# Kernel tuning notes

Hardware: AMD Instinct MI355X
Metric: run time of the kernel (lower is better)

Reference implementation:

```python
import jax, jax.numpy as jnp
import numpy as np

C, H1, H2, K, HOUT = 128, 4, 5, 3, 4  # h_dim, gat1 heads, gat2 heads, BAN k, BAN h_out
BN_EPS = 1e-5


def _gat(x, W, a_src, a_dst, bias, src, dst, mask, N):
    # PyG-style GATConv: x:[N,Fin], W:[Fin,H*C], a_*:[H,C], mask:[E] (1=valid edge)
    H, Ch = a_src.shape
    xh = (x @ W).reshape(N, H, Ch)
    es = jnp.einsum('nhc,hc->nh', xh, a_src)
    ed = jnp.einsum('nhc,hc->nh', xh, a_dst)
    e = jax.nn.leaky_relu(es[src] + ed[dst], 0.2)                      # [E,H]
    e = jnp.where(mask[:, None] > 0, e, -1e9)
    m = jax.ops.segment_max(e, dst, num_segments=N)                    # [N,H]
    p = jnp.exp(e - m[dst]) * mask[:, None]
    s = jax.ops.segment_sum(p, dst, num_segments=N)
    alpha = p / s[dst]                                                 # segment softmax over incoming edges
    out = jax.ops.segment_sum(xh[src] * alpha[:, :, None], dst, num_segments=N)
    return out.reshape(N, H * Ch) + bias


def _forward(cell_features, Wd, bd, W1, a1s, a1d, b1, Wl1, bl1, W2, a2s, a2d, b2, Wl2, bl2,
             Wfc, bfc, Whg, bhg, Wc, bc, Wv, bv, Wq, bq, h_mat, h_bias, bn_gamma, bn_beta,
             triplets, edge_index):
    N = triplets.shape[0]
    src0, dst0 = edge_index[0], edge_index[1]
    # clean_edge_index drops self loops; GATConv (PyG default) re-adds exactly one per node
    idx = jnp.arange(N, dtype=src0.dtype)
    src = jnp.concatenate([src0, idx])
    dst = jnp.concatenate([dst0, idx])
    mask = jnp.concatenate([(src0 != dst0).astype(jnp.float32), jnp.ones((N,), jnp.float32)])
    x = triplets[:, :4].astype(jnp.float32) @ Wd + bd                  # drug_linear
    h1 = jax.nn.elu(_gat(x, W1, a1s, a1d, b1, src, dst, mask, N)) @ Wl1 + bl1
    h2 = jax.nn.elu(_gat(h1, W2, a2s, a2d, b2, src, dst, mask, N)) @ Wl2 + bl2
    h = jnp.mean(h1 + h2, axis=0)                                      # [C] graph readout
    hg = jax.nn.relu(h @ Wfc + bfc) @ Whg + bhg                        # [C]
    c = jax.nn.relu(cell_features @ Wc + bc)                           # [B,C]
    B = c.shape[0]
    v = jnp.broadcast_to(hg, (B, C))
    # BANLayer (DrugBAN) with singleton v/q sequence length
    v_ = jax.nn.relu(v @ Wv + bv)                                      # [B,C*K]
    q_ = jax.nn.relu(c @ Wq + bq)
    att = jnp.einsum('hk,bk,bk->bh', h_mat, v_, q_) + h_bias           # [B,HOUT]
    fused = att.sum(axis=1, keepdims=True) * (v_ * q_)                 # sum over heads of bilinear pooling
    logits = fused.reshape(B, C, K).sum(axis=-1)                       # AvgPool1d(k)*k == group sum
    mu = logits.mean(axis=0)
    var = logits.var(axis=0)                                           # biased var, as torch BN
    return (logits - mu) / jnp.sqrt(var + BN_EPS) * bn_gamma + bn_beta


def setup_inputs():
    key = jax.random.key(0)
    ks = iter(jax.random.split(key, 40))
    N, E, B, CF = 20000, 500000, 256, 954
    def w(shape, fan):
        return jax.random.normal(next(ks), shape, jnp.float32) / np.sqrt(fan)
    return dict(
        cell_features=jax.random.normal(next(ks), (B, CF), jnp.float32),
        Wd=w((4, C), 4), bd=jnp.zeros((C,), jnp.float32),
        W1=w((C, H1 * C), C), a1s=w((H1, C), C), a1d=w((H1, C), C), b1=jnp.zeros((H1 * C,), jnp.float32),
        Wl1=w((H1 * C, C), H1 * C), bl1=jnp.zeros((C,), jnp.float32),
        W2=w((C, H2 * C), C), a2s=w((H2, C), C), a2d=w((H2, C), C), b2=jnp.zeros((H2 * C,), jnp.float32),
        Wl2=w((H2 * C, C), H2 * C), bl2=jnp.zeros((C,), jnp.float32),
        Wfc=w((C, 2 * C), C), bfc=jnp.zeros((2 * C,), jnp.float32),
        Whg=w((2 * C, C), 2 * C), bhg=jnp.zeros((C,), jnp.float32),
        Wc=w((CF, C), CF), bc=jnp.zeros((C,), jnp.float32),
        Wv=w((C, C * K), C), bv=jnp.zeros((C * K,), jnp.float32),
        Wq=w((C, C * K), C), bq=jnp.zeros((C * K,), jnp.float32),
        h_mat=w((HOUT, C * K), C * K), h_bias=jnp.zeros((HOUT,), jnp.float32),
        bn_gamma=jnp.ones((C,), jnp.float32), bn_beta=jnp.zeros((C,), jnp.float32),
        triplets=jax.random.randint(next(ks), (N, 4), 0, 10, dtype=jnp.int32),
        edge_index=jax.random.randint(next(ks), (2, E), 0, N, dtype=jnp.int32),
    )


def reference(cell_features, Wd, bd, W1, a1s, a1d, b1, Wl1, bl1, W2, a2s, a2d, b2, Wl2, bl2,
              Wfc, bfc, Whg, bhg, Wc, bc, Wv, bv, Wq, bq, h_mat, h_bias, bn_gamma, bn_beta,
              triplets, edge_index):
    return _forward(cell_features, Wd, bd, W1, a1s, a1d, b1, Wl1, bl1, W2, a2s, a2d, b2, Wl2, bl2,
                    Wfc, bfc, Whg, bhg, Wc, bc, Wv, bv, Wq, bq, h_mat, h_bias, bn_gamma, bn_beta,
                    triplets, edge_index)
```

## Files before the change

kernel.cpp:

```cpp
#include <hip/hip_runtime.h>
#include <hip/hip_bf16.h>
#include <math.h>

#define CDIV(a,b) (((a)+(b)-1)/(b))

typedef __attribute__((ext_vector_type(8))) short short8v;
typedef __attribute__((ext_vector_type(4))) float f32x4;

__device__ inline float bf2lo(unsigned u) { return __uint_as_float(u << 16); }
__device__ inline float bf2hi(unsigned u) { return __uint_as_float(u & 0xffff0000u); }
__device__ inline float leaky(float v) { return v > 0.f ? v : 0.2f * v; }

__global__ void k_prep(const float* __restrict__ W1, __hip_bfloat16* __restrict__ W1t,
                       const float* __restrict__ Wl1, __hip_bfloat16* __restrict__ Wl1t,
                       const float* __restrict__ W2, __hip_bfloat16* __restrict__ W2t,
                       const float* __restrict__ Wl2, __hip_bfloat16* __restrict__ Wl2t,
                       const float* __restrict__ Wc, float* __restrict__ Wct,
                       const float* __restrict__ Wq, float* __restrict__ Wqt,
                       float* __restrict__ colsum, int* __restrict__ degz,
                       float* __restrict__ esz, int N) {
  int i = blockIdx.x * 256 + threadIdx.x;
  const int n1 = 128 * 512, n2 = 512 * 128, n3 = 128 * 640, n4 = 640 * 128;
  const int n5 = 954 * 128, n6 = 128 * 384;
  if (i < n1) { int m = i / 128, k = i % 128; W1t[i] = __float2bfloat16(W1[(size_t)k * 512 + m]); return; }
  i -= n1;
  if (i < n2) { int m = i / 512, k = i % 512; Wl1t[i] = __float2bfloat16(Wl1[(size_t)k * 128 + m]); return; }
  i -= n2;
  if (i < n3) { int m = i / 128, k = i % 128; W2t[i] = __float2bfloat16(W2[(size_t)k * 640 + m]); return; }
  i -= n3;
  if (i < n4) { int m = i / 640, k = i % 640; Wl2t[i] = __float2bfloat16(Wl2[(size_t)k * 128 + m]); return; }
  i -= n4;
  if (i < n5) { int m = i / 954, k = i % 954; Wct[i] = Wc[(size_t)k * 128 + m]; return; }
  i -= n5;
  if (i < n6) { int m = i / 128, k = i % 128; Wqt[i] = Wq[(size_t)k * 384 + m]; return; }
  i -= n6;
  if (i < 128) { colsum[i] = 0.f; return; }
  i -= 128;
  if (i < 2 * N) { degz[i] = 0; return; }
  i -= 2 * N;
  if (i < 18 * N) { esz[i] = 0.f; return; }
}

__global__ void k_degdrug(const int* __restrict__ src0, const int* __restrict__ dst0,
                          int* __restrict__ deg, int E,
                          const int* __restrict__ trip, const float* __restrict__ Wd,
                          const float* __restrict__ bd, __hip_bfloat16* __restrict__ x,
                          int N) {
  int i = blockIdx.x * 256 + threadIdx.x;
  if (i < E) {
    int s = src0[i], d = dst0[i];
    if (s != d) atomicAdd(&deg[d], 1);
    return;
  }
  i -= E;
  if (i >= N * 128) return;
  int n = i >> 7, c = i & 127;
  const int* t = trip + n * 4;
  float acc = bd[c];
  acc += (float)t[0] * Wd[c] + (float)t[1] * Wd[128 + c] +
         (float)t[2] * Wd[256 + c] + (float)t[3] * Wd[384 + c];
  x[i] = __float2bfloat16(acc);
}

template <bool BIAS, bool COLSUM, bool COEF>
__global__ void k_gemm_mfma(const __hip_bfloat16* __restrict__ A,
                            const __hip_bfloat16* __restrict__ Bt,
                            const float* __restrict__ bias,
                            __hip_bfloat16* __restrict__ Cb,
                            float* __restrict__ colsum,
                            const float* __restrict__ as_, const float* __restrict__ ad_,
                            float* __restrict__ es, float* __restrict__ ed,
                            int Nr, int K, int M) {
  __shared__ short As[64 * 40];
  __shared__ short Bs[64 * 40];
  int tid = threadIdx.x;
  int lane = tid & 63, wid = tid >> 6;
  int wr = wid >> 1, wc = wid & 1;
  int lrow = lane & 15;
  int row0 = blockIdx.y * 64, col0 = blockIdx.x * 64;

  int arow = tid >> 2, akc = tid & 3;
  int grow = row0 + arow; if (grow >= Nr) grow = Nr - 1;
  const __hip_bfloat16* agp = A + (size_t)grow * K + akc * 8;
  const __hip_bfloat16* bgp = Bt + (size_t)(col0 + arow) * K + akc * 8;
  short* asp = &As[arow * 40 + akc * 8];
  short* bsp = &Bs[arow * 40 + akc * 8];

  f32x4 acc00 = {0.f,0.f,0.f,0.f}, acc01 = acc00, acc10 = acc00, acc11 = acc00;

  int lkc = lane >> 4;
  const short* a0p = &As[(wr * 32 + lrow) * 40 + lkc * 8];
  const short* a1p = &As[(wr * 32 + 16 + lrow) * 40 + lkc * 8];
  const short* b0p = &Bs[(wc * 32 + lrow) * 40 + lkc * 8];
  const short* b1p = &Bs[(wc * 32 + 16 + lrow) * 40 + lkc * 8];

  short8v av = *(const short8v*)agp;
  short8v bv = *(const short8v*)bgp;
  for (int k0 = 0; k0 < K; k0 += 32) {
    __syncthreads();
    *(short8v*)asp = av;
    *(short8v*)bsp = bv;
    __syncthreads();
    if (k0 + 32 < K) {
      av = *(const short8v*)(agp + k0 + 32);
      bv = *(const short8v*)(bgp + k0 + 32);
    }
    short8v a0 = *(const short8v*)a0p;
    short8v a1 = *(const short8v*)a1p;
    short8v b0 = *(const short8v*)b0p;
    short8v b1 = *(const short8v*)b1p;
    acc00 = __builtin_amdgcn_mfma_f32_16x16x32_bf16(a0, b0, acc00, 0, 0, 0);
    acc01 = __builtin_amdgcn_mfma_f32_16x16x32_bf16(a0, b1, acc01, 0, 0, 0);
    acc10 = __builtin_amdgcn_mfma_f32_16x16x32_bf16(a1, b0, acc10, 0, 0, 0);
    acc11 = __builtin_amdgcn_mfma_f32_16x16x32_bf16(a1, b1, acc11, 0, 0, 0);
  }

  int rbase = row0 + wr * 32 + (lane >> 4) * 4;
  int cbase = col0 + wc * 32 + lrow;
  int hplane = col0 >> 7;
  float part0 = 0.f, part1 = 0.f;
  float esp[2][4], edp[2][4];
  float as0, as1, ad0, ad1;
  if (COEF) {
#pragma unroll
    for (int m = 0; m < 2; ++m)
#pragma unroll
      for (int r = 0; r < 4; ++r) { esp[m][r] = 0.f; edp[m][r] = 0.f; }
    int ch0 = (cbase & 127);
    as0 = as_[hplane * 128 + ch0];
    as1 = as_[hplane * 128 + ch0 + 16];
    ad0 = ad_[hplane * 128 + ch0];
    ad1 = ad_[hplane * 128 + ch0 + 16];
  }
#pragma unroll
  for (int m = 0; m < 2; ++m) {
#pragma unroll
    for (int n = 0; n < 2; ++n) {
      f32x4 acc = m == 0 ? (n == 0 ? acc00 : acc01) : (n == 0 ? acc10 : acc11);
      int col = cbase + n * 16;
      int plane = col >> 7, ch = col & 127;
      float bv2 = BIAS ? bias[col] : 0.f;
      __hip_bfloat16* cp = Cb + (size_t)plane * Nr * 128 + ch;
#pragma unroll
      for (int r = 0; r < 4; ++r) {
        int grow2 = rbase + m * 16 + r;
        if (grow2 >= Nr) continue;
        float v = acc[r] + bv2;
        cp[(size_t)grow2 * 128] = __float2bfloat16(v);
        if (COLSUM) { if (n == 0) part0 += v; else part1 += v; }
        if (COEF) {
          esp[m][r] += v * (n == 0 ? as0 : as1);
          edp[m][r] += v * (n == 0 ? ad0 : ad1);
        }
      }
    }
  }
  if (COLSUM) {
    part0 += __shfl_xor(part0, 16); part0 += __shfl_xor(part0, 32);
    part1 += __shfl_xor(part1, 16); part1 += __shfl_xor(part1, 32);
    if (lane < 16) {
      atomicAdd(&colsum[cbase], part0);
      atomicAdd(&colsum[cbase + 16], part1);
    }
  }
  if (COEF) {
#pragma unroll
    for (int m = 0; m < 2; ++m) {
#pragma unroll
      for (int r = 0; r < 4; ++r) {
        float e = esp[m][r], d = edp[m][r];
        e += __shfl_xor(e, 1); e += __shfl_xor(e, 2);
        e += __shfl_xor(e, 4); e += __shfl_xor(e, 8);
        d += __shfl_xor(d, 1); d += __shfl_xor(d, 2);
        d += __shfl_xor(d, 4); d += __shfl_xor(d, 8);
        if ((lane & 15) == 0) {
          int grow2 = rbase + m * 16 + r;
          if (grow2 < Nr) {
            atomicAdd(&es[(size_t)hplane * Nr + grow2], e);
            atomicAdd(&ed[(size_t)hplane * Nr + grow2], d);
          }
        }
      }
    }
  }
}

__global__ void k_dotmm(const float* __restrict__ A, const float* __restrict__ Bt,
                        const float* __restrict__ bias, float* __restrict__ C,
                        int Nr, int K, int M) {
  int wid = (blockIdx.x * blockDim.x + threadIdx.x) >> 6;
  int lane = threadIdx.x & 63;
  if (wid >= Nr * M) return;
  int b = wid / M, m = wid % M;
  const float* ar = A + (size_t)b * K;
  const float* br = Bt + (size_t)m * K;
  float acc = 0.f;
  for (int k = lane * 2; k + 1 < K; k += 128) {
    float2 av = *(const float2*)(ar + k);
    float2 bv = *(const float2*)(br + k);
    acc += av.x * bv.x + av.y * bv.y;
  }
#pragma unroll
  for (int off = 32; off; off >>= 1) acc += __shfl_xor(acc, off);
  if (lane == 0) C[wid] = fmaxf(acc + bias[m], 0.f);
}

__global__ void k_scan(const int* __restrict__ deg, int* __restrict__ rowptr, int N) {
  __shared__ int part[1024];
  int t = threadIdx.x;
  int chunk = (N + 1023) >> 10;
  int b0 = t * chunk, b1 = min(N, b0 + chunk);
  int s = 0;
  for (int i = b0; i < b1; i++) s += deg[i];
  part[t] = s;
  __syncthreads();
  for (int off = 1; off < 1024; off <<= 1) {
    int v = (t >= off) ? part[t - off] : 0;
    __syncthreads();
    part[t] += v;
    __syncthreads();
  }
  int run = (t == 0) ? 0 : part[t - 1];
  for (int i = b0; i < b1; i++) { rowptr[i] = run; run += deg[i]; }
  if (b1 == N) rowptr[N] = run;
}

__global__ void k_fill_adj(const int* __restrict__ src0, const int* __restrict__ dst0,
                           const int* __restrict__ rowptr, int* __restrict__ cursor,
                           int* __restrict__ adj, int E) {
  int e = blockIdx.x * 256 + threadIdx.x;
  if (e >= E) return;
  int s = src0[e], d = dst0[e];
  if (s != d) {
    int pos = rowptr[d] + atomicAdd(&cursor[d], 1);
    adj[pos] = s;
  }
}

__device__ __forceinline__ void acc8p(const char* xbase, int loff, unsigned pk, int j,
                                      float& a0, float& a1) {
  unsigned k0 = __builtin_amdgcn_readlane(pk, j);
  unsigned k1 = __builtin_amdgcn_readlane(pk, j + 1);
  unsigned k2 = __builtin_amdgcn_readlane(pk, j + 2);
  unsigned k3 = __builtin_amdgcn_readlane(pk, j + 3);
  unsigned k4 = __builtin_amdgcn_readlane(pk, j + 4);
  unsigned k5 = __builtin_amdgcn_readlane(pk, j + 5);
  unsigned k6 = __builtin_amdgcn_readlane(pk, j + 6);
  unsigned k7 = __builtin_amdgcn_readlane(pk, j + 7);
  unsigned u0 = *(const unsigned*)(xbase + (size_t)(k0 & 0x7FFFu) * 256 + loff);
  unsigned u1 = *(const unsigned*)(xbase + (size_t)(k1 & 0x7FFFu) * 256 + loff);
  unsigned u2 = *(const unsigned*)(xbase + (size_t)(k2 & 0x7FFFu) * 256 + loff);
  unsigned u3 = *(const unsigned*)(xbase + (size_t)(k3 & 0x7FFFu) * 256 + loff);
  unsigned u4 = *(const unsigned*)(xbase + (size_t)(k4 & 0x7FFFu) * 256 + loff);
  unsigned u5 = *(const unsigned*)(xbase + (size_t)(k5 & 0x7FFFu) * 256 + loff);
  unsigned u6 = *(const unsigned*)(xbase + (size_t)(k6 & 0x7FFFu) * 256 + loff);
  unsigned u7 = *(const unsigned*)(xbase + (size_t)(k7 & 0x7FFFu) * 256 + loff);
  float p0 = __uint_as_float(k0 & 0xFFFF0000u);
  float p1 = __uint_as_float(k1 & 0xFFFF0000u);
  float p2 = __uint_as_float(k2 & 0xFFFF0000u);
  float p3 = __uint_as_float(k3 & 0xFFFF0000u);
  float p4 = __uint_as_float(k4 & 0xFFFF0000u);
  float p5 = __uint_as_float(k5 & 0xFFFF0000u);
  float p6 = __uint_as_float(k6 & 0xFFFF0000u);
  float p7 = __uint_as_float(k7 & 0xFFFF0000u);
  a0 += p0 * bf2lo(u0); a1 += p0 * bf2hi(u0);
  a0 += p1 * bf2lo(u1); a1 += p1 * bf2hi(u1);
  a0 += p2 * bf2lo(u2); a1 += p2 * bf2hi(u2);
  a0 += p3 * bf2lo(u3); a1 += p3 * bf2hi(u3);
  a0 += p4 * bf2lo(u4); a1 += p4 * bf2hi(u4);
  a0 += p5 * bf2lo(u5); a1 += p5 * bf2hi(u5);
  a0 += p6 * bf2lo(u6); a1 += p6 * bf2hi(u6);
  a0 += p7 * bf2lo(u7); a1 += p7 * bf2hi(u7);
}

__global__ void k_gat_gather(const int* __restrict__ rowptr, const int* __restrict__ adj,
                             const float* __restrict__ es, const float* __restrict__ ed,
                             const __hip_bfloat16* __restrict__ xh,
                             const float* __restrict__ bias,
                             __hip_bfloat16* __restrict__ gout, int N, int H) {
  int nb = gridDim.x, bx = blockIdx.x;
  int sb = ((nb & 7) == 0) ? ((bx & 7) * (nb >> 3) + (bx >> 3)) : bx;
  int h = blockIdx.y;
  int n = sb * 4 + (threadIdx.x >> 6);
  int lane = threadIdx.x & 63;
  if (n >= N) return;
  int base = rowptr[n];
  int deg = rowptr[n + 1] - base;
  const float* esh = es + (size_t)h * N;
  float edn = ed[(size_t)h * N + n];
  float vself = leaky(esh[n] + edn);
  const char* xbase = (const char*)xh + (size_t)h * N * 256;
  int loff = lane * 4;

  float a0 = 0.f, a1 = 0.f;
  float psum = 0.f, pself, m;

  if (deg <= 64) {
    int s = 0; float v = -3e38f;
    if (lane < deg) { s = adj[base + lane]; v = leaky(esh[s] + edn); }
    m = fmaxf(vself, v);
#pragma unroll
    for (int off = 32; off; off >>= 1) m = fmaxf(m, __shfl_xor(m, off));
    float p = (lane < deg) ? __expf(v - m) : 0.f;
    pself = __expf(vself - m);
    psum = p;
    unsigned pk = (__float_as_uint(p) & 0xFFFF0000u) | (unsigned)s;
    for (int j = 0; j < deg; j += 8) acc8p(xbase, loff, pk, j, a0, a1);
  } else {
    m = vself;
    for (int i = lane; i < deg; i += 64) {
      int s = adj[base + i];
      m = fmaxf(m, leaky(esh[s] + edn));
    }
#pragma unroll
    for (int off = 32; off; off >>= 1) m = fmaxf(m, __shfl_xor(m, off));
    pself = __expf(vself - m);
    for (int c = 0; c < deg; c += 64) {
      int i = c + lane;
      int s = 0; float p = 0.f;
      if (i < deg) {
        s = adj[base + i];
        p = __expf(leaky(esh[s] + edn) - m);
        psum += p;
      }
      unsigned pk = (__float_as_uint(p) & 0xFFFF0000u) | (unsigned)s;
      int cnt = min(64, deg - c);
      for (int j = 0; j < cnt; j += 8) acc8p(xbase, loff, pk, j, a0, a1);
    }
  }

  {
    unsigned u = *(const unsigned*)(xbase + (size_t)n * 256 + loff);
    a0 += pself * bf2lo(u);
    a1 += pself * bf2hi(u);
  }
#pragma unroll
  for (int off = 32; off; off >>= 1) psum += __shfl_xor(psum, off);
  psum += pself;
  float inv = 1.f / psum;
  float2 bv = ((const float2*)(bias + h * 128))[lane];
  float o0 = a0 * inv + bv.x;
  float o1 = a1 * inv + bv.y;
  o0 = o0 > 0.f ? o0 : __expf(o0) - 1.f;
  o1 = o1 > 0.f ? o1 : __expf(o1) - 1.f;
  __hip_bfloat162 r;
  r.x = __float2bfloat16(o0);
  r.y = __float2bfloat16(o1);
  ((__hip_bfloat162*)(gout + (size_t)n * (H * 128) + h * 128))[lane] = r;
}

__global__ void k_head(const float* __restrict__ colsum, const float* __restrict__ Wfc,
                       const float* __restrict__ bfc, const float* __restrict__ Whg,
                       const float* __restrict__ bhg, const float* __restrict__ Wv,
                       const float* __restrict__ bv, float* __restrict__ vvec, float invN) {
  __shared__ float h[128], t1[256], hg[128];
  int t = threadIdx.x;
  if (t < 128) h[t] = colsum[t] * invN;
  __syncthreads();
  float acc = bfc[t];
  for (int k = 0; k < 128; k++) acc += h[k] * Wfc[k * 256 + t];
  t1[t] = fmaxf(acc, 0.f);
  __syncthreads();
  if (t < 128) {
    float a2 = bhg[t];
    for (int k = 0; k < 256; k++) a2 += t1[k] * Whg[k * 128 + t];
    hg[t] = a2;
  }
  __syncthreads();
  for (int j = t; j < 384; j += 256) {
    float a3 = bv[j];
    for (int k = 0; k < 128; k++) a3 += hg[k] * Wv[k * 384 + j];
    vvec[j] = fmaxf(a3, 0.f);
  }
}

__global__ void k_fused(const float* __restrict__ vvec, const float* __restrict__ q,
                        const float* __restrict__ hmat, const float* __restrict__ hbias,
                        float* __restrict__ logits) {
  int b = blockIdx.x, c = threadIdx.x;
  __shared__ float red[128];
  float t[3];
  float part = 0.f;
#pragma unroll
  for (int j = 0; j < 3; j++) {
    int k = c * 3 + j;
    float hs = hmat[k] + hmat[384 + k] + hmat[768 + k] + hmat[1152 + k];
    t[j] = vvec[k] * q[(size_t)b * 384 + k];
    part += hs * t[j];
  }
  red[c] = part;
  __syncthreads();
  for (int s = 64; s > 0; s >>= 1) {
    if (c < s) red[c] += red[c + s];
    __syncthreads();
  }
  float attsum = red[0] + (hbias[0] + hbias[1] + hbias[2] + hbias[3]);
  logits[(size_t)b * 128 + c] = attsum * (t[0] + t[1] + t[2]);
}

__global__ void k_bn(const float* __restrict__ logits, const float* __restrict__ gamma,
                     const float* __restrict__ beta, float* __restrict__ out, int B) {
  int c = blockIdx.x, b = threadIdx.x;
  __shared__ float s1[256], s2[256];
  float v = logits[(size_t)b * 128 + c];
  s1[b] = v; s2[b] = v * v;
  __syncthreads();
  for (int s = B / 2; s > 0; s >>= 1) {
    if (b < s) { s1[b] += s1[b + s]; s2[b] += s2[b + s]; }
    __syncthreads();
  }
  float mu = s1[0] / B;
  float var = s2[0] / B - mu * mu;
  out[(size_t)b * 128 + c] = (v - mu) * rsqrtf(var + 1e-5f) * gamma[c] + beta[c];
}

extern "C" void kernel_launch(void* const* d_in, const int* in_sizes, int n_in,
                              void* d_out, int out_size, void* d_ws, size_t ws_size,
                              hipStream_t stream) {
  const float* cell = (const float*)d_in[0];
  const float* Wd   = (const float*)d_in[1];
  const float* bd   = (const float*)d_in[2];
  const float* W1   = (const float*)d_in[3];
  const float* a1s  = (const float*)d_in[4];
  const float* a1d  = (const float*)d_in[5];
  const float* b1   = (const float*)d_in[6];
  const float* Wl1  = (const float*)d_in[7];
  const float* bl1  = (const float*)d_in[8];
  const float* W2   = (const float*)d_in[9];
  const float* a2s  = (const float*)d_in[10];
  const float* a2d  = (const float*)d_in[11];
  const float* b2   = (const float*)d_in[12];
  const float* Wl2  = (const float*)d_in[13];
  const float* bl2  = (const float*)d_in[14];
  const float* Wfc  = (const float*)d_in[15];
  const float* bfc  = (const float*)d_in[16];
  const float* Whg  = (const float*)d_in[17];
  const float* bhg  = (const float*)d_in[18];
  const float* Wc   = (const float*)d_in[19];
  const float* bc   = (const float*)d_in[20];
  const float* Wv   = (const float*)d_in[21];
  const float* bv   = (const float*)d_in[22];
  const float* Wq   = (const float*)d_in[23];
  const float* bq   = (const float*)d_in[24];
  const float* hmat = (const float*)d_in[25];
  const float* hbias= (const float*)d_in[26];
  const float* gamma= (const float*)d_in[27];
  const float* beta = (const float*)d_in[28];
  const int* trip   = (const int*)d_in[29];
  const int* eidx   = (const int*)d_in[30];

  const int N = in_sizes[29] / 4;
  const int E = in_sizes[30] / 2;
  const int B = in_sizes[0] / 954;
  float* out = (float*)d_out;

  __hip_bfloat16* xb    = (__hip_bfloat16*)d_ws;
  __hip_bfloat16* xhb   = xb + (size_t)N * 128;
  __hip_bfloat16* goutb = xhb + (size_t)N * 640;
  __hip_bfloat16* h1b   = goutb + (size_t)N * 640;
  __hip_bfloat16* h2b   = h1b + (size_t)N * 128;
  __hip_bfloat16* W1t   = h2b + (size_t)N * 128;
  __hip_bfloat16* Wl1t  = W1t + 512 * 128;
  __hip_bfloat16* W2t   = Wl1t + 128 * 512;
  __hip_bfloat16* Wl2t  = W2t + 640 * 128;
  float* es1    = (float*)(Wl2t + 128 * 640);
  float* ed1    = es1 + (size_t)4 * N;
  float* es2    = ed1 + (size_t)4 * N;
  float* ed2    = es2 + (size_t)5 * N;
  float* colsum = ed2 + (size_t)5 * N;
  float* cbuf   = colsum + 128;
  float* qbuf   = cbuf + (size_t)B * 128;
  float* vvec   = qbuf + (size_t)B * 384;
  float* logits = vvec + 384;
  float* Wct    = logits + (size_t)B * 128;
  float* Wqt    = Wct + 128 * 954;
  int* rowptr   = (int*)(Wqt + 384 * 128);
  int* degb     = rowptr + (N + 1);
  int* cursor   = degb + N;
  int* adj      = cursor + N;

  const int* src0 = eidx;
  const int* dst0 = eidx + E;

  {
    int tot = 128*512 + 512*128 + 128*640 + 640*128 + 954*128 + 128*384
              + 128 + 2 * N + 18 * N;
    k_prep<<<CDIV(tot, 256), 256, 0, stream>>>(W1, W1t, Wl1, Wl1t, W2, W2t, Wl2, Wl2t,
                                               Wc, Wct, Wq, Wqt, colsum, degb, es1, N);
  }

  k_degdrug<<<CDIV(E + N * 128, 256), 256, 0, stream>>>(src0, dst0, degb, E,
                                                        trip, Wd, bd, xb, N);
  k_scan<<<1, 1024, 0, stream>>>(degb, rowptr, N);
  k_fill_adj<<<CDIV(E, 256), 256, 0, stream>>>(src0, dst0, rowptr, cursor, adj, E);

  {
    dim3 g(512 / 64, CDIV(N, 64));
    k_gemm_mfma<false, false, true><<<g, 256, 0, stream>>>(
        xb, W1t, nullptr, xhb, nullptr, a1s, a1d, es1, ed1, N, 128, 512);
  }
  {
    dim3 g(CDIV(N, 4), 4);
    k_gat_gather<<<g, 256, 0, stream>>>(rowptr, adj, es1, ed1, xhb, b1, goutb, N, 4);
  }
  {
    dim3 g(128 / 64, CDIV(N, 64));
    k_gemm_mfma<true, true, false><<<g, 256, 0, stream>>>(
        goutb, Wl1t, bl1, h1b, colsum, nullptr, nullptr, nullptr, nullptr, N, 512, 128);
  }

  {
    dim3 g(640 / 64, CDIV(N, 64));
    k_gemm_mfma<false, false, true><<<g, 256, 0, stream>>>(
        h1b, W2t, nullptr, xhb, nullptr, a2s, a2d, es2, ed2, N, 128, 640);
  }
  {
    dim3 g(CDIV(N, 4), 5);
    k_gat_gather<<<g, 256, 0, stream>>>(rowptr, adj, es2, ed2, xhb, b2, goutb, N, 5);
  }
  {
    dim3 g(128 / 64, CDIV(N, 64));
    k_gemm_mfma<true, true, false><<<g, 256, 0, stream>>>(
        goutb, Wl2t, bl2, h2b, colsum, nullptr, nullptr, nullptr, nullptr, N, 640, 128);
  }

  k_head<<<1, 256, 0, stream>>>(colsum, Wfc, bfc, Whg, bhg, Wv, bv, vvec, 1.0f / N);
  k_dotmm<<<CDIV(B * 128, 4), 256, 0, stream>>>(cell, Wct, bc, cbuf, B, 954, 128);
  k_dotmm<<<CDIV(B * 384, 4), 256, 0, stream>>>(cbuf, Wqt, bq, qbuf, B, 128, 384);
  k_fused<<<B, 128, 0, stream>>>(vvec, qbuf, hmat, hbias, logits);
  k_bn<<<128, B, 0, stream>>>(logits, gamma, beta, out, B);
}
```

Measured before the change: 475.6 us.

## Process all attention heads per node in one GAT gather block

The GAT gather kernel is templated on the head count, so one wavefront handles every head of a node instead of launching one block per head. Adjacency indices and the broadcast source index are loaded once and shared across heads, with per-head attention weights packed as bf16 halves into three lane registers. This cuts redundant adjacency and rowptr reads and launch work. In exchange it raises register pressure, lowers the number of blocks, and unrolls by two edges instead of eight.

```diff
diff --git a/kernel.cpp b/kernel.cpp
--- a/kernel.cpp
+++ b/kernel.cpp
@@ -237,116 +237,153 @@
   }
 }
 
-__device__ __forceinline__ void acc8p(const char* xbase, int loff, unsigned pk, int j,
-                                      float& a0, float& a1) {
-  unsigned k0 = __builtin_amdgcn_readlane(pk, j);
-  unsigned k1 = __builtin_amdgcn_readlane(pk, j + 1);
-  unsigned k2 = __builtin_amdgcn_readlane(pk, j + 2);
-  unsigned k3 = __builtin_amdgcn_readlane(pk, j + 3);
-  unsigned k4 = __builtin_amdgcn_readlane(pk, j + 4);
-  unsigned k5 = __builtin_amdgcn_readlane(pk, j + 5);
-  unsigned k6 = __builtin_amdgcn_readlane(pk, j + 6);
-  unsigned k7 = __builtin_amdgcn_readlane(pk, j + 7);
-  unsigned u0 = *(const unsigned*)(xbase + (size_t)(k0 & 0x7FFFu) * 256 + loff);
-  unsigned u1 = *(const unsigned*)(xbase + (size_t)(k1 & 0x7FFFu) * 256 + loff);
-  unsigned u2 = *(const unsigned*)(xbase + (size_t)(k2 & 0x7FFFu) * 256 + loff);
-  unsigned u3 = *(const unsigned*)(xbase + (size_t)(k3 & 0x7FFFu) * 256 + loff);
-  unsigned u4 = *(const unsigned*)(xbase + (size_t)(k4 & 0x7FFFu) * 256 + loff);
-  unsigned u5 = *(const unsigned*)(xbase + (size_t)(k5 & 0x7FFFu) * 256 + loff);
-  unsigned u6 = *(const unsigned*)(xbase + (size_t)(k6 & 0x7FFFu) * 256 + loff);
-  unsigned u7 = *(const unsigned*)(xbase + (size_t)(k7 & 0x7FFFu) * 256 + loff);
-  float p0 = __uint_as_float(k0 & 0xFFFF0000u);
-  float p1 = __uint_as_float(k1 & 0xFFFF0000u);
-  float p2 = __uint_as_float(k2 & 0xFFFF0000u);
-  float p3 = __uint_as_float(k3 & 0xFFFF0000u);
-  float p4 = __uint_as_float(k4 & 0xFFFF0000u);
-  float p5 = __uint_as_float(k5 & 0xFFFF0000u);
-  float p6 = __uint_as_float(k6 & 0xFFFF0000u);
-  float p7 = __uint_as_float(k7 & 0xFFFF0000u);
-  a0 += p0 * bf2lo(u0); a1 += p0 * bf2hi(u0);
-  a0 += p1 * bf2lo(u1); a1 += p1 * bf2hi(u1);
-  a0 += p2 * bf2lo(u2); a1 += p2 * bf2hi(u2);
-  a0 += p3 * bf2lo(u3); a1 += p3 * bf2hi(u3);
-  a0 += p4 * bf2lo(u4); a1 += p4 * bf2hi(u4);
-  a0 += p5 * bf2lo(u5); a1 += p5 * bf2hi(u5);
-  a0 += p6 * bf2lo(u6); a1 += p6 * bf2hi(u6);
-  a0 += p7 * bf2lo(u7); a1 += p7 * bf2hi(u7);
-}
-
+template <int H>
+__device__ __forceinline__ void accE(const char* xbase, size_t plane, int loff,
+                                     unsigned ks, unsigned k01, unsigned k23,
+                                     float a[H][2]) {
+  size_t row = (size_t)(ks & 0x7FFFu) * 256 + loff;
+  float p[H];
+  p[0] = __uint_as_float(k01 & 0xFFFF0000u);
+  if (H > 1) p[1] = __uint_as_float(k01 << 16);
+  if (H > 2) p[2] = __uint_as_float(k23 & 0xFFFF0000u);
+  if (H > 3) p[3] = __uint_as_float(k23 << 16);
+  if (H > 4) p[4] = __uint_as_float(ks & 0xFFFF0000u);
+#pragma unroll
+  for (int h = 0; h < H; ++h) {
+    unsigned u = *(const unsigned*)(xbase + (size_t)h * plane + row);
+    a[h][0] += p[h] * bf2lo(u);
+    a[h][1] += p[h] * bf2hi(u);
+  }
+}
+
+template <int H>
 __global__ void k_gat_gather(const int* __restrict__ rowptr, const int* __restrict__ adj,
                              const float* __restrict__ es, const float* __restrict__ ed,
                              const __hip_bfloat16* __restrict__ xh,
                              const float* __restrict__ bias,
-                             __hip_bfloat16* __restrict__ gout, int N, int H) {
+                             __hip_bfloat16* __restrict__ gout, int N) {
   int nb = gridDim.x, bx = blockIdx.x;
   int sb = ((nb & 7) == 0) ? ((bx & 7) * (nb >> 3) + (bx >> 3)) : bx;
-  int h = blockIdx.y;
   int n = sb * 4 + (threadIdx.x >> 6);
   int lane = threadIdx.x & 63;
   if (n >= N) return;
   int base = rowptr[n];
   int deg = rowptr[n + 1] - base;
-  const float* esh = es + (size_t)h * N;
-  float edn = ed[(size_t)h * N + n];
-  float vself = leaky(esh[n] + edn);
-  const char* xbase = (const char*)xh + (size_t)h * N * 256;
+  const char* xbase = (const char*)xh;
+  const size_t plane = (size_t)N * 256;
   int loff = lane * 4;
 
-  float a0 = 0.f, a1 = 0.f;
-  float psum = 0.f, pself, m;
+  float edn[H], vself[H], pself[H], psum[H];
+  float a[H][2];
+#pragma unroll
+  for (int h = 0; h < H; ++h) {
+    edn[h] = ed[(size_t)h * N + n];
+    vself[h] = leaky(es[(size_t)h * N + n] + edn[h]);
+    a[h][0] = 0.f; a[h][1] = 0.f;
+    psum[h] = 0.f;
+  }
 
   if (deg <= 64) {
-    int s = 0; float v = -3e38f;
-    if (lane < deg) { s = adj[base + lane]; v = leaky(esh[s] + edn); }
-    m = fmaxf(vself, v);
-#pragma unroll
-    for (int off = 32; off; off >>= 1) m = fmaxf(m, __shfl_xor(m, off));
-    float p = (lane < deg) ? __expf(v - m) : 0.f;
-    pself = __expf(vself - m);
-    psum = p;
-    unsigned pk = (__float_as_uint(p) & 0xFFFF0000u) | (unsigned)s;
-    for (int j = 0; j < deg; j += 8) acc8p(xbase, loff, pk, j, a0, a1);
+    int s = 0; bool val = lane < deg;
+    if (val) s = adj[base + lane];
+    float p[H];
+#pragma unroll
+    for (int h = 0; h < H; ++h) {
+      float v = val ? leaky(es[(size_t)h * N + s] + edn[h]) : -3e38f;
+      float mh = fmaxf(vself[h], v);
+#pragma unroll
+      for (int off = 32; off; off >>= 1) mh = fmaxf(mh, __shfl_xor(mh, off));
+      p[h] = val ? __expf(v - mh) : 0.f;
+      pself[h] = __expf(vself[h] - mh);
+      psum[h] = p[h];
+    }
+    unsigned ks = (unsigned)s;
+    if (H > 4) ks |= (__float_as_uint(p[H > 4 ? 4 : 0]) & 0xFFFF0000u);
+    unsigned k01 = (__float_as_uint(p[0]) & 0xFFFF0000u);
+    if (H > 1) k01 |= (__float_as_uint(p[1]) >> 16);
+    unsigned k23 = 0;
+    if (H > 2) k23 = (__float_as_uint(p[2]) & 0xFFFF0000u);
+    if (H > 3) k23 |= (__float_as_uint(p[3]) >> 16);
+    for (int j = 0; j < deg; j += 2) {
+      unsigned ks0 = __builtin_amdgcn_readlane(ks, j);
+      unsigned k010 = __builtin_amdgcn_readlane(k01, j);
+      unsigned k230 = __builtin_amdgcn_readlane(k23, j);
+      unsigned ks1 = __builtin_amdgcn_readlane(ks, j + 1);
+      unsigned k011 = __builtin_amdgcn_readlane(k01, j + 1);
+      unsigned k231 = __builtin_amdgcn_readlane(k23, j + 1);
+      accE<H>(xbase, plane, loff, ks0, k010, k230, a);
+      accE<H>(xbase, plane, loff, ks1, k011, k231, a);
+    }
   } else {
-    m = vself;
+    float mh[H];
+#pragma unroll
+    for (int h = 0; h < H; ++h) mh[h] = vself[h];
     for (int i = lane; i < deg; i += 64) {
       int s = adj[base + i];
-      m = fmaxf(m, leaky(esh[s] + edn));
-    }
-#pragma unroll
-    for (int off = 32; off; off >>= 1) m = fmaxf(m, __shfl_xor(m, off));
-    pself = __expf(vself - m);
+#pragma unroll
+      for (int h = 0; h < H; ++h)
+        mh[h] = fmaxf(mh[h], leaky(es[(size_t)h * N + s] + edn[h]));
+    }
+#pragma unroll
+    for (int h = 0; h < H; ++h) {
+#pragma unroll
+      for (int off = 32; off; off >>= 1) mh[h] = fmaxf(mh[h], __shfl_xor(mh[h], off));
+      pself[h] = __expf(vself[h] - mh[h]);
+    }
     for (int c = 0; c < deg; c += 64) {
       int i = c + lane;
-      int s = 0; float p = 0.f;
+      int s = 0; float p[H];
+#pragma unroll
+      for (int h = 0; h < H; ++h) p[h] = 0.f;
       if (i < deg) {
         s = adj[base + i];
-        p = __expf(leaky(esh[s] + edn) - m);
-        psum += p;
+#pragma unroll
+        for (int h = 0; h < H; ++h) {
+          p[h] = __expf(leaky(es[(size_t)h * N + s] + edn[h]) - mh[h]);
+          psum[h] += p[h];
+        }
       }
-      unsigned pk = (__float_as_uint(p) & 0xFFFF0000u) | (unsigned)s;
+      unsigned ks = (unsigned)s;
+      if (H > 4) ks |= (__float_as_uint(p[H > 4 ? 4 : 0]) & 0xFFFF0000u);
+      unsigned k01 = (__float_as_uint(p[0]) & 0xFFFF0000u);
+      if (H > 1) k01 |= (__float_as_uint(p[1]) >> 16);
+      unsigned k23 = 0;
+      if (H > 2) k23 = (__float_as_uint(p[2]) & 0xFFFF0000u);
+      if (H > 3) k23 |= (__float_as_uint(p[3]) >> 16);
       int cnt = min(64, deg - c);
-      for (int j = 0; j < cnt; j += 8) acc8p(xbase, loff, pk, j, a0, a1);
-    }
-  }
-
-  {
-    unsigned u = *(const unsigned*)(xbase + (size_t)n * 256 + loff);
-    a0 += pself * bf2lo(u);
-    a1 += pself * bf2hi(u);
-  }
-#pragma unroll
-  for (int off = 32; off; off >>= 1) psum += __shfl_xor(psum, off);
-  psum += pself;
-  float inv = 1.f / psum;
-  float2 bv = ((const float2*)(bias + h * 128))[lane];
-  float o0 = a0 * inv + bv.x;
-  float o1 = a1 * inv + bv.y;
-  o0 = o0 > 0.f ? o0 : __expf(o0) - 1.f;
-  o1 = o1 > 0.f ? o1 : __expf(o1) - 1.f;
-  __hip_bfloat162 r;
-  r.x = __float2bfloat16(o0);
-  r.y = __float2bfloat16(o1);
-  ((__hip_bfloat162*)(gout + (size_t)n * (H * 128) + h * 128))[lane] = r;
+      for (int j = 0; j < cnt; j += 2) {
+        unsigned ks0 = __builtin_amdgcn_readlane(ks, j);
+        unsigned k010 = __builtin_amdgcn_readlane(k01, j);
+        unsigned k230 = __builtin_amdgcn_readlane(k23, j);
+        unsigned ks1 = __builtin_amdgcn_readlane(ks, j + 1);
+        unsigned k011 = __builtin_amdgcn_readlane(k01, j + 1);
+        unsigned k231 = __builtin_amdgcn_readlane(k23, j + 1);
+        accE<H>(xbase, plane, loff, ks0, k010, k230, a);
+        accE<H>(xbase, plane, loff, ks1, k011, k231, a);
+      }
+    }
+  }
+
+#pragma unroll
+  for (int h = 0; h < H; ++h) {
+    unsigned u = *(const unsigned*)(xbase + (size_t)h * plane + (size_t)n * 256 + loff);
+    a[h][0] += pself[h] * bf2lo(u);
+    a[h][1] += pself[h] * bf2hi(u);
+    float ps = psum[h];
+#pragma unroll
+    for (int off = 32; off; off >>= 1) ps += __shfl_xor(ps, off);
+    ps += pself[h];
+    float inv = 1.f / ps;
+    float2 bv = ((const float2*)(bias + h * 128))[lane];
+    float o0 = a[h][0] * inv + bv.x;
+    float o1 = a[h][1] * inv + bv.y;
+    o0 = o0 > 0.f ? o0 : __expf(o0) - 1.f;
+    o1 = o1 > 0.f ? o1 : __expf(o1) - 1.f;
+    __hip_bfloat162 r;
+    r.x = __float2bfloat16(o0);
+    r.y = __float2bfloat16(o1);
+    ((__hip_bfloat162*)(gout + (size_t)n * (H * 128) + h * 128))[lane] = r;
+  }
 }
 
 __global__ void k_head(const float* __restrict__ colsum, const float* __restrict__ Wfc,
@@ -499,10 +536,7 @@
     k_gemm_mfma<false, false, true><<<g, 256, 0, stream>>>(
         xb, W1t, nullptr, xhb, nullptr, a1s, a1d, es1, ed1, N, 128, 512);
   }
-  {
-    dim3 g(CDIV(N, 4), 4);
-    k_gat_gather<<<g, 256, 0, stream>>>(rowptr, adj, es1, ed1, xhb, b1, goutb, N, 4);
-  }
+  k_gat_gather<4><<<CDIV(N, 4), 256, 0, stream>>>(rowptr, adj, es1, ed1, xhb, b1, goutb, N);
   {
     dim3 g(128 / 64, CDIV(N, 64));
     k_gemm_mfma<true, true, false><<<g, 256, 0, stream>>>(
@@ -514,10 +548,7 @@
     k_gemm_mfma<false, false, true><<<g, 256, 0, stream>>>(
         h1b, W2t, nullptr, xhb, nullptr, a2s, a2d, es2, ed2, N, 128, 640);
   }
-  {
-    dim3 g(CDIV(N, 4), 5);
-    k_gat_gather<<<g, 256, 0, stream>>>(rowptr, adj, es2, ed2, xhb, b2, goutb, N, 5);
-  }
+  k_gat_gather<5><<<CDIV(N, 4), 256, 0, stream>>>(rowptr, adj, es2, ed2, xhb, b2, goutb, N);
   {
     dim3 g(128 / 64, CDIV(N, 64));
     k_gemm_mfma<true, true, false><<<g, 256, 0, stream>>>(
```

New measurement: 516.0 us. 1.09x slower.
